# Optimization experiments

Hardware: AMD Instinct MI355X
Metric: run time of the kernel (lower is better)

The kernel has to match this reference:

```python
import jax, jax.numpy as jnp
import numpy as np
from jax import lax

FILTERS = 64

def _conv(a, k):
    # NHWC input, HWIO kernel, SAME padding, stride 1
    return lax.conv_general_dilated(a, k, window_strides=(1, 1), padding='SAME',
                                    dimension_numbers=('NHWC', 'HWIO', 'NHWC'))

def _hard_sigmoid(z):
    # Keras ConvLSTM2D default recurrent_activation
    return jnp.clip(0.2 * z + 0.5, 0.0, 1.0)

def setup_inputs() -> dict:
    key = jax.random.key(0)
    k1, k2, k3 = jax.random.split(key, 3)
    B, T, H, W, C = 8, 16, 96, 96, 8
    x = jax.random.normal(k1, (B, T, H, W, C), dtype=jnp.float32)
    Wx = jax.random.normal(k2, (3, 3, C, 4 * FILTERS), dtype=jnp.float32) * 0.05
    Wh = jax.random.normal(k3, (3, 3, FILTERS, 4 * FILTERS), dtype=jnp.float32) * 0.05
    b = jnp.zeros((4 * FILTERS,), dtype=jnp.float32)
    return {"x": x, "Wx": Wx, "Wh": Wh, "b": b}

def reference(x, Wx, Wh, b):
    # Keras ConvLSTM2D forward (inference: dropout off), return_sequences=False.
    B, T, H, W, C = x.shape
    F = Wh.shape[2]

    def step(carry, xt):
        h, c = carry
        z = _conv(xt, Wx) + _conv(h, Wh) + b  # (B,H,W,4F)
        i, f, g, o = jnp.split(z, 4, axis=-1)  # Keras gate order i,f,c,o
        i = _hard_sigmoid(i)
        f = _hard_sigmoid(f)
        o = _hard_sigmoid(o)
        c_new = f * c + i * jnp.tanh(g)
        h_new = o * jnp.tanh(c_new)
        return (h_new, c_new), None

    h0 = jnp.zeros((B, H, W, F), x.dtype)
    xs = jnp.moveaxis(x, 1, 0)  # (T,B,H,W,C)
    (h, c), _ = lax.scan(step, (h0, h0), xs)
    return h  # (B,H,W,F)
```

## Files before the change

kernel.cpp:

```cpp
#include <hip/hip_runtime.h>
#include <cmath>


#define HTOT 96
#define WTOT 96
#define CINX 8
#define FF   64
#define G4   256
#define BB   8
#define TT   16
#define HP   72
#define NPOS (BB*HTOT*WTOT)

typedef __attribute__((ext_vector_type(8))) short short8;
typedef __attribute__((ext_vector_type(4))) float floatx4;

union U16 { uint4 u; short8 s; };

__device__ __forceinline__ float hsig(float z) {
    return fminf(fmaxf(0.2f * z + 0.5f, 0.f), 1.f);
}

__device__ __forceinline__ float ftanh(float x) {
    float e = __expf(-2.f * fabsf(x));
    float t = (1.f - e) / (1.f + e);
    return copysignf(t, x);
}

__device__ __forceinline__ ushort f2bf(float f) {
    unsigned u = __float_as_uint(f);
    u = (u + 0x7fff + ((u >> 16) & 1)) >> 16;
    return (ushort)u;
}

__device__ __forceinline__ void async16(const uint4* g, uint4* l) {
    __builtin_amdgcn_global_load_lds(
        (const __attribute__((address_space(1))) void*)g,
        (__attribute__((address_space(3))) void*)l, 16, 0, 0);
}

__global__ __launch_bounds__(256) void conv_x_bf16(const float* __restrict__ x,
                                                   ushort* __restrict__ xbf, int n4) {
    int i = blockIdx.x * 256 + threadIdx.x;
    if (i >= n4) return;
    float4 v = ((const float4*)x)[i];
    ushort4 o;
    o.x = f2bf(v.x); o.y = f2bf(v.y); o.z = f2bf(v.z); o.w = f2bf(v.w);
    ((ushort4*)xbf)[i] = o;
}

__global__ __launch_bounds__(256) void prep_w(const float* __restrict__ Wx,
                                              const float* __restrict__ Wh,
                                              ushort* __restrict__ Bp) {
    int idx = blockIdx.x * 256 + threadIdx.x;
    if (idx >= 4 * 21 * 256) return;
    int lane = idx & 63;
    int g = (idx >> 6) & 3;
    int rest = idx >> 8;
    int s = rest % 21, slice = rest / 21;
    int q = lane >> 4, col = lane & 15;
    int n = g * 64 + slice * 16 + col;
    ushort o[8];
    if (s < 18) {
        int tap = s >> 1;
        int cbase = (s & 1) * 32 + q * 8;
        #pragma unroll
        for (int j = 0; j < 8; ++j)
            o[j] = f2bf(Wh[((size_t)tap * FF + cbase + j) * G4 + n]);
    } else {
        int tap = (s - 18) * 4 + q;
        #pragma unroll
        for (int j = 0; j < 8; ++j)
            o[j] = (tap < 9) ? f2bf(Wx[((size_t)tap * CINX + j) * G4 + n]) : (ushort)0;
    }
    U16 u;
    #pragma unroll
    for (int j = 0; j < 8; ++j) ((ushort*)&u)[j] = o[j];
    ((uint4*)Bp)[idx] = u.u;
}

__global__ __launch_bounds__(256, 4) void convlstm_mfma(
    const ushort* __restrict__ xbf, int t,
    const ushort* __restrict__ hS_in,
    ushort* __restrict__ hS_out,
    float* __restrict__ cS,
    const ushort* __restrict__ Bp,
    const float* __restrict__ bias,
    float* __restrict__ out, int last)
{
    __shared__ __align__(16) ushort hpatch[180 * HP];
    __shared__ uint4 bslab[3 * 256];

    const int tid = threadIdx.x;
    const int x0 = blockIdx.x * 8, y0 = blockIdx.y * 16;
    const int bb = blockIdx.z >> 2, slice = blockIdx.z & 3;

    const uint4* Bp4 = (const uint4*)Bp;
    const uint4* src = Bp4 + (size_t)(slice * 21) * 256;

    async16(src + tid,       &bslab[tid]);
    async16(src + 256 + tid, &bslab[256 + tid]);

    for (int e = tid; e < 1440; e += 256) {
        int part = e / 180, pp = e - part * 180;
        int py = pp / 10, px = pp - py * 10;
        int gy = y0 - 1 + py, gx = x0 - 1 + px;
        uint4 v = make_uint4(0, 0, 0, 0);
        if (gy >= 0 && gy < HTOT && gx >= 0 && gx < WTOT) {
            int s8 = part >> 1, half = part & 1;
            size_t gpos = ((size_t)bb * HTOT + gy) * WTOT + gx;
            v = *(const uint4*)(hS_in + ((size_t)s8 * NPOS + gpos) * 16 + half * 8);
        }
        *(uint4*)(hpatch + pp * HP + part * 8) = v;
    }
    if (tid < 180) {
        int py = tid / 10, px = tid - py * 10;
        int gy = y0 - 1 + py, gx = x0 - 1 + px;
        uint4 v = make_uint4(0, 0, 0, 0);
        if (gy >= 0 && gy < HTOT && gx >= 0 && gx < WTOT)
            v = *(const uint4*)(xbf + ((((size_t)bb * TT + t) * HTOT + gy) * WTOT + gx) * CINX);
        *(uint4*)(hpatch + tid * HP + 64) = v;
    }

    const int w = tid >> 6, lane = tid & 63, q = lane >> 4, col = lane & 15;

    int pos0[2];
    #pragma unroll
    for (int mt = 0; mt < 2; ++mt)
        pos0[mt] = (w * 4 + mt * 2 + (col >> 3)) * 10 + (col & 7);

    floatx4 acc[2][4];
    #pragma unroll
    for (int g = 0; g < 4; ++g) {
        float bv = bias[g * 64 + slice * 16 + col];
        acc[0][g] = (floatx4){bv, bv, bv, bv};
        acc[1][g] = (floatx4){bv, bv, bv, bv};
    }

    __syncthreads();

    #pragma unroll
    for (int s = 0; s < 21; ++s) {
        if (s + 2 < 21)
            async16(src + (s + 2) * 256 + tid, &bslab[((s + 2) % 3) * 256 + tid]);
        const uint4* slab = &bslab[(s % 3) * 256];
        U16 b4[4], a4[2];
        #pragma unroll
        for (int g = 0; g < 4; ++g)
            b4[g].u = slab[g * 64 + lane];
        if (s < 18) {
            int tap = s >> 1, kh = s & 1;
            int dy = tap / 3, dx = tap - 3 * dy;
            #pragma unroll
            for (int mt = 0; mt < 2; ++mt)
                a4[mt].u = *(const uint4*)(hpatch + (pos0[mt] + dy * 10 + dx) * HP + kh * 32 + q * 8);
        } else {
            int tap = (s - 18) * 4 + q; if (tap > 8) tap = 8;
            int dy = tap / 3, dx = tap - 3 * dy;
            #pragma unroll
            for (int mt = 0; mt < 2; ++mt)
                a4[mt].u = *(const uint4*)(hpatch + (pos0[mt] + dy * 10 + dx) * HP + 64);
        }
        #pragma unroll
        for (int mt = 0; mt < 2; ++mt)
            #pragma unroll
            for (int g = 0; g < 4; ++g)
                acc[mt][g] = __builtin_amdgcn_mfma_f32_16x16x32_bf16(a4[mt].s, b4[g].s, acc[mt][g], 0, 0, 0);
        if (s < 20) {
            if (s < 19) asm volatile("s_waitcnt vmcnt(1)" ::: "memory");
            else        asm volatile("s_waitcnt vmcnt(0)" ::: "memory");
            __builtin_amdgcn_s_barrier();
            __builtin_amdgcn_sched_barrier(0);
        }
    }

    #pragma unroll
    for (int mt = 0; mt < 2; ++mt) {
        #pragma unroll
        for (int r = 0; r < 4; ++r) {
            int m = w * 32 + mt * 16 + q * 4 + r;
            int gy = y0 + (m >> 3), gx = x0 + (m & 7);
            size_t gpos = ((size_t)bb * HTOT + gy) * WTOT + gx;
            size_t idx = ((size_t)slice * NPOS + gpos) * 16 + col;
            float zi = acc[mt][0][r], zf = acc[mt][1][r];
            float zg = acc[mt][2][r], zo = acc[mt][3][r];
            float cn = hsig(zf) * cS[idx] + hsig(zi) * ftanh(zg);
            cS[idx] = cn;
            float hn = hsig(zo) * ftanh(cn);
            hS_out[idx] = f2bf(hn);
            if (last) out[gpos * 64 + slice * 16 + col] = hn;
        }
    }
}

extern "C" void kernel_launch(void* const* d_in, const int* in_sizes, int n_in,
                              void* d_out, int out_size, void* d_ws, size_t ws_size,
                              hipStream_t stream) {
    const float* x  = (const float*)d_in[0];
    const float* Wx = (const float*)d_in[1];
    const float* Wh = (const float*)d_in[2];
    const float* b  = (const float*)d_in[3];

    const size_t NX = (size_t)BB * TT * HTOT * WTOT * CINX;
    const size_t NH = (size_t)NPOS * FF;

    char* ws = (char*)d_ws;
    ushort* xbf = (ushort*)ws;                  ws += NX * 2;
    ushort* hS0 = (ushort*)ws;                  ws += NH * 2;
    ushort* hS1 = (ushort*)ws;                  ws += NH * 2;
    float*  cS  = (float*)ws;                   ws += NH * 4;
    ushort* Bp  = (ushort*)ws;

    hipMemsetAsync(hS0, 0, NH * 2, stream);
    hipMemsetAsync(cS,  0, NH * 4, stream);

    conv_x_bf16<<<(int)((NX / 4 + 255) / 256), 256, 0, stream>>>(x, xbf, (int)(NX / 4));
    prep_w<<<(4 * 21 * 256 + 255) / 256, 256, 0, stream>>>(Wx, Wh, Bp);

    dim3 grid(WTOT / 8, HTOT / 16, BB * 4);
    for (int t = 0; t < TT; ++t) {
        const ushort* hin = (t & 1) ? hS1 : hS0;
        ushort* hout      = (t & 1) ? hS0 : hS1;
        convlstm_mfma<<<grid, 256, 0, stream>>>(xbf, t, hin, hout, cS, Bp, b,
                                                (float*)d_out, t == TT - 1);
    }
}
```

Before: 700.3 us.

## Retile ConvLSTM step to 16x12 with planar LDS halo and A-fragment reuse

Each block now covers a 16-wide by 12-tall tile instead of 8x16, and each wave computes three rows of 16 pixels. The h and x halo is loaded into planar LDS buffers with async global-to-LDS copies, using clamped addresses and a zero pad buffer in place of the earlier synchronous register-staged copy. The weight slabs are reordered so that, for each dx and channel half, A fragments loaded for successive dy taps are reused across output rows through a small rotating register window. This cuts LDS reads and halo overhead per output and overlaps the halo load, at the cost of more accumulator registers and more complex indexing.

```diff
diff --git a/kernel.cpp b/kernel.cpp
--- a/kernel.cpp
+++ b/kernel.cpp
@@ -9,7 +9,6 @@
 #define G4   256
 #define BB   8
 #define TT   16
-#define HP   72
 #define NPOS (BB*HTOT*WTOT)
 
 typedef __attribute__((ext_vector_type(8))) short short8;
@@ -33,7 +32,7 @@
     return (ushort)u;
 }
 
-__device__ __forceinline__ void async16(const uint4* g, uint4* l) {
+__device__ __forceinline__ void async16(const void* g, void* l) {
     __builtin_amdgcn_global_load_lds(
         (const __attribute__((address_space(1))) void*)g,
         (__attribute__((address_space(3))) void*)l, 16, 0, 0);
@@ -62,8 +61,10 @@
     int n = g * 64 + slice * 16 + col;
     ushort o[8];
     if (s < 18) {
-        int tap = s >> 1;
-        int cbase = (s & 1) * 32 + q * 8;
+        int dxw = s / 6, rem = s - 6 * dxw;
+        int khw = rem / 3, dyw = rem - 3 * khw;
+        int tap = dyw * 3 + dxw;
+        int cbase = khw * 32 + q * 8;
         #pragma unroll
         for (int j = 0; j < 8; ++j)
             o[j] = f2bf(Wh[((size_t)tap * FF + cbase + j) * G4 + n]);
@@ -86,100 +87,121 @@
     float* __restrict__ cS,
     const ushort* __restrict__ Bp,
     const float* __restrict__ bias,
+    const uint4* __restrict__ zpad,
     float* __restrict__ out, int last)
 {
-    __shared__ __align__(16) ushort hpatch[180 * HP];
-    __shared__ uint4 bslab[3 * 256];
+    __shared__ __align__(16) ushort hplanes[8 * 2048];
+    __shared__ __align__(16) ushort xplane[2048];
+    __shared__ __align__(16) uint4  bslab[3 * 256];
 
     const int tid = threadIdx.x;
-    const int x0 = blockIdx.x * 8, y0 = blockIdx.y * 16;
+    const int x0 = blockIdx.x * 16, y0 = blockIdx.y * 12;
     const int bb = blockIdx.z >> 2, slice = blockIdx.z & 3;
 
-    const uint4* Bp4 = (const uint4*)Bp;
-    const uint4* src = Bp4 + (size_t)(slice * 21) * 256;
-
-    async16(src + tid,       &bslab[tid]);
-    async16(src + 256 + tid, &bslab[256 + tid]);
-
-    for (int e = tid; e < 1440; e += 256) {
-        int part = e / 180, pp = e - part * 180;
-        int py = pp / 10, px = pp - py * 10;
+    const uint4* gB = (const uint4*)Bp + (size_t)(slice * 21) * 256 + tid;
+    async16(gB,       &bslab[tid]);
+    async16(gB + 256, &bslab[256 + tid]);
+
+    {
+        int py = tid / 18, px = tid - py * 18;
         int gy = y0 - 1 + py, gx = x0 - 1 + px;
-        uint4 v = make_uint4(0, 0, 0, 0);
-        if (gy >= 0 && gy < HTOT && gx >= 0 && gx < WTOT) {
-            int s8 = part >> 1, half = part & 1;
-            size_t gpos = ((size_t)bb * HTOT + gy) * WTOT + gx;
-            v = *(const uint4*)(hS_in + ((size_t)s8 * NPOS + gpos) * 16 + half * 8);
-        }
-        *(uint4*)(hpatch + pp * HP + part * 8) = v;
-    }
-    if (tid < 180) {
-        int py = tid / 10, px = tid - py * 10;
-        int gy = y0 - 1 + py, gx = x0 - 1 + px;
-        uint4 v = make_uint4(0, 0, 0, 0);
-        if (gy >= 0 && gy < HTOT && gx >= 0 && gx < WTOT)
-            v = *(const uint4*)(xbf + ((((size_t)bb * TT + t) * HTOT + gy) * WTOT + gx) * CINX);
-        *(uint4*)(hpatch + tid * HP + 64) = v;
+        bool ok = (gy >= 0 && gy < HTOT && gx >= 0 && gx < WTOT);
+        int gyc = gy < 0 ? 0 : (gy > HTOT - 1 ? HTOT - 1 : gy);
+        int gxc = gx < 0 ? 0 : (gx > WTOT - 1 ? WTOT - 1 : gx);
+        size_t gpos = ((size_t)bb * HTOT + gyc) * WTOT + gxc;
+        #pragma unroll
+        for (int p = 0; p < 8; ++p) {
+            const void* src = ok
+                ? (const void*)(hS_in + ((size_t)(p >> 1) * NPOS + gpos) * 16 + (p & 1) * 8)
+                : (const void*)zpad;
+            async16(src, hplanes + p * 2048 + tid * 8);
+        }
+        const void* sxp = ok
+            ? (const void*)(xbf + ((((size_t)bb * TT + t) * HTOT + gyc) * WTOT + gxc) * CINX)
+            : (const void*)zpad;
+        async16(sxp, xplane + tid * 8);
     }
 
     const int w = tid >> 6, lane = tid & 63, q = lane >> 4, col = lane & 15;
-
-    int pos0[2];
-    #pragma unroll
-    for (int mt = 0; mt < 2; ++mt)
-        pos0[mt] = (w * 4 + mt * 2 + (col >> 3)) * 10 + (col & 7);
-
-    floatx4 acc[2][4];
+    const int rowb = w * 3;
+
+    const ushort* hA = hplanes + q * 2048 + (rowb * 18 + col) * 8;
+    const uint4*  bA = bslab + lane;
+
+    floatx4 acc[3][4];
     #pragma unroll
     for (int g = 0; g < 4; ++g) {
         float bv = bias[g * 64 + slice * 16 + col];
         acc[0][g] = (floatx4){bv, bv, bv, bv};
         acc[1][g] = (floatx4){bv, bv, bv, bv};
+        acc[2][g] = (floatx4){bv, bv, bv, bv};
     }
 
     __syncthreads();
 
-    #pragma unroll
-    for (int s = 0; s < 21; ++s) {
-        if (s + 2 < 21)
-            async16(src + (s + 2) * 256 + tid, &bslab[((s + 2) % 3) * 256 + tid]);
-        const uint4* slab = &bslab[(s % 3) * 256];
-        U16 b4[4], a4[2];
-        #pragma unroll
-        for (int g = 0; g < 4; ++g)
-            b4[g].u = slab[g * 64 + lane];
-        if (s < 18) {
-            int tap = s >> 1, kh = s & 1;
-            int dy = tap / 3, dx = tap - 3 * dy;
+    U16 aw[4];
+    #pragma unroll
+    for (int dx = 0; dx < 3; ++dx) {
+        #pragma unroll
+        for (int kh = 0; kh < 2; ++kh) {
             #pragma unroll
-            for (int mt = 0; mt < 2; ++mt)
-                a4[mt].u = *(const uint4*)(hpatch + (pos0[mt] + dy * 10 + dx) * HP + kh * 32 + q * 8);
-        } else {
-            int tap = (s - 18) * 4 + q; if (tap > 8) tap = 8;
-            int dy = tap / 3, dx = tap - 3 * dy;
+            for (int j = 0; j < 3; ++j)
+                aw[j].u = *(const uint4*)(hA + kh * 8192 + j * 144 + dx * 8);
             #pragma unroll
-            for (int mt = 0; mt < 2; ++mt)
-                a4[mt].u = *(const uint4*)(hpatch + (pos0[mt] + dy * 10 + dx) * HP + 64);
-        }
-        #pragma unroll
-        for (int mt = 0; mt < 2; ++mt)
+            for (int dy = 0; dy < 3; ++dy) {
+                const int s = dx * 6 + kh * 3 + dy;
+                if (dy)
+                    aw[(dy + 2) & 3].u = *(const uint4*)(hA + kh * 8192 + (dy + 2) * 144 + dx * 8);
+                async16(gB + (s + 2) * 256, &bslab[((dy + 2) % 3) * 256 + tid]);
+                #pragma unroll
+                for (int g = 0; g < 4; ++g) {
+                    U16 b4; b4.u = bA[dy * 256 + g * 64];
+                    #pragma unroll
+                    for (int mt = 0; mt < 3; ++mt)
+                        acc[mt][g] = __builtin_amdgcn_mfma_f32_16x16x32_bf16(
+                            aw[(mt + dy) & 3].s, b4.s, acc[mt][g], 0, 0, 0);
+                }
+                asm volatile("s_waitcnt vmcnt(1)" ::: "memory");
+                __builtin_amdgcn_s_barrier();
+                __builtin_amdgcn_sched_barrier(0);
+            }
+        }
+    }
+    #pragma unroll
+    for (int sx = 0; sx < 3; ++sx) {
+        int tap = sx * 4 + q; if (tap > 8) tap = 8;
+        int dyq = tap / 3, dxq = tap - 3 * dyq;
+        const ushort* xA = xplane + ((rowb + dyq) * 18 + col + dxq) * 8;
+        if (sx == 0) async16(gB + 20 * 256, &bslab[2 * 256 + tid]);
+        U16 a4[3];
+        #pragma unroll
+        for (int mt = 0; mt < 3; ++mt)
+            a4[mt].u = *(const uint4*)(xA + mt * 144);
+        #pragma unroll
+        for (int g = 0; g < 4; ++g) {
+            U16 b4; b4.u = bA[sx * 256 + g * 64];
             #pragma unroll
-            for (int g = 0; g < 4; ++g)
-                acc[mt][g] = __builtin_amdgcn_mfma_f32_16x16x32_bf16(a4[mt].s, b4[g].s, acc[mt][g], 0, 0, 0);
-        if (s < 20) {
-            if (s < 19) asm volatile("s_waitcnt vmcnt(1)" ::: "memory");
-            else        asm volatile("s_waitcnt vmcnt(0)" ::: "memory");
+            for (int mt = 0; mt < 3; ++mt)
+                acc[mt][g] = __builtin_amdgcn_mfma_f32_16x16x32_bf16(
+                    a4[mt].s, b4.s, acc[mt][g], 0, 0, 0);
+        }
+        if (sx == 0) {
+            asm volatile("s_waitcnt vmcnt(1)" ::: "memory");
             __builtin_amdgcn_s_barrier();
             __builtin_amdgcn_sched_barrier(0);
-        }
-    }
-
-    #pragma unroll
-    for (int mt = 0; mt < 2; ++mt) {
+        } else if (sx == 1) {
+            asm volatile("s_waitcnt vmcnt(0)" ::: "memory");
+            __builtin_amdgcn_s_barrier();
+            __builtin_amdgcn_sched_barrier(0);
+        }
+    }
+
+    #pragma unroll
+    for (int mt = 0; mt < 3; ++mt) {
+        int gy = y0 + rowb + mt;
         #pragma unroll
         for (int r = 0; r < 4; ++r) {
-            int m = w * 32 + mt * 16 + q * 4 + r;
-            int gy = y0 + (m >> 3), gx = x0 + (m & 7);
+            int gx = x0 + q * 4 + r;
             size_t gpos = ((size_t)bb * HTOT + gy) * WTOT + gx;
             size_t idx = ((size_t)slice * NPOS + gpos) * 16 + col;
             float zi = acc[mt][0][r], zf = acc[mt][1][r];
@@ -209,19 +231,21 @@
     ushort* hS0 = (ushort*)ws;                  ws += NH * 2;
     ushort* hS1 = (ushort*)ws;                  ws += NH * 2;
     float*  cS  = (float*)ws;                   ws += NH * 4;
-    ushort* Bp  = (ushort*)ws;
+    ushort* Bp  = (ushort*)ws;                  ws += (size_t)4*21*256*16;
+    uint4*  zpad = (uint4*)ws;
 
     hipMemsetAsync(hS0, 0, NH * 2, stream);
     hipMemsetAsync(cS,  0, NH * 4, stream);
+    hipMemsetAsync(zpad, 0, 64, stream);
 
     conv_x_bf16<<<(int)((NX / 4 + 255) / 256), 256, 0, stream>>>(x, xbf, (int)(NX / 4));
     prep_w<<<(4 * 21 * 256 + 255) / 256, 256, 0, stream>>>(Wx, Wh, Bp);
 
-    dim3 grid(WTOT / 8, HTOT / 16, BB * 4);
+    dim3 grid(WTOT / 16, HTOT / 12, BB * 4);
     for (int t = 0; t < TT; ++t) {
         const ushort* hin = (t & 1) ? hS1 : hS0;
         ushort* hout      = (t & 1) ? hS0 : hS1;
-        convlstm_mfma<<<grid, 256, 0, stream>>>(xbf, t, hin, hout, cS, Bp, b,
+        convlstm_mfma<<<grid, 256, 0, stream>>>(xbf, t, hin, hout, cS, Bp, b, zpad,
                                                 (float*)d_out, t == TT - 1);
     }
 }
```

Result: faster. 587.7 us (-16.1%).
